# Optimization experiments

Hardware: AMD Instinct MI355X
Metric: run time of the kernel (lower is better)

## Reference

```python
import math
import jax, jax.numpy as jnp
import numpy as np

B, L, C, H = 32, 320, 768, 12
LENS_T = 64
KEEP_RATIO = 0.7
AD_H = 64   # Mixer adapter bottleneck width (assumed bottleneck adapter)
EPS = 1e-5  # torch LayerNorm default


def _ln(x, g, b):
    m = jnp.mean(x, axis=-1, keepdims=True)
    v = jnp.mean((x - m) ** 2, axis=-1, keepdims=True)
    return (x - m) * jax.lax.rsqrt(v + EPS) * g + b


def _attention(x, qkv_w, proj_w, proj_b):
    b, l, c = x.shape
    dh = c // H
    qkv = (x @ qkv_w).reshape(b, l, 3, H, dh)
    q = jnp.transpose(qkv[:, :, 0], (0, 2, 1, 3))  # [B,H,L,Dh]
    k = jnp.transpose(qkv[:, :, 1], (0, 2, 1, 3))
    v = jnp.transpose(qkv[:, :, 2], (0, 2, 1, 3))
    a = jax.nn.softmax(jnp.einsum('bhid,bhjd->bhij', q * (dh ** -0.5), k), axis=-1)
    out = jnp.einsum('bhij,bhjd->bhid', a, v).transpose(0, 2, 1, 3).reshape(b, l, c)
    return out @ proj_w + proj_b, a


def _mixer(x, dw, db, uw, ub):
    return jax.nn.gelu(x @ dw + db, approximate=False) @ uw + ub


def _mlp(x, w1, b1, w2, b2):
    return jax.nn.gelu(x @ w1 + b1, approximate=False) @ w2 + b2


def _ce(attn, tokens, lens_t, lens_keep, gidx):
    # attn: [B,H,Lt+Ls,Lt+Ls]; average template->search block over heads and template rows
    attn_t = jnp.mean(attn[:, :, :lens_t, lens_t:], axis=(1, 2))  # [B, Ls]
    order = jnp.argsort(-attn_t, axis=1)                          # descending sort indices
    topk_idx, rest_idx = order[:, :lens_keep], order[:, lens_keep:]
    keep = jnp.take_along_axis(gidx, topk_idx, axis=1)
    removed = jnp.take_along_axis(gidx, rest_idx, axis=1)
    kept_tok = jnp.take_along_axis(tokens[:, lens_t:], topk_idx[..., None], axis=1)
    return jnp.concatenate([tokens[:, :lens_t], kept_tok], axis=1), keep, removed


def setup_inputs():
    key = jax.random.key(0)
    ks = jax.random.split(key, 12)
    p = lambda k, shape: jax.random.normal(k, shape, jnp.float32) * 0.02
    ls = L - LENS_T
    return {
        'x': jax.random.normal(ks[0], (B, L, C), jnp.float32),
        'xi': jax.random.normal(ks[1], (B, L, C), jnp.float32),
        'gi_t': jnp.arange(B * LENS_T, dtype=jnp.int32).reshape(B, LENS_T),
        'gi_ti': jnp.arange(B * LENS_T, dtype=jnp.int32).reshape(B, LENS_T),
        'gi_s': jnp.arange(B * ls, dtype=jnp.int32).reshape(B, ls),
        'gi_si': jnp.arange(B * ls, dtype=jnp.int32).reshape(B, ls),
        'layer': 0,
        'n1_g': jnp.ones((C,), jnp.float32), 'n1_b': jnp.zeros((C,), jnp.float32),
        'qkv_w': p(ks[2], (C, 3 * C)),
        'proj_w': p(ks[3], (C, C)), 'proj_b': jnp.zeros((C,), jnp.float32),
        'n2_g': jnp.ones((C,), jnp.float32), 'n2_b': jnp.zeros((C,), jnp.float32),
        'fc1_w': p(ks[4], (C, 4 * C)), 'fc1_b': jnp.zeros((4 * C,), jnp.float32),
        'fc2_w': p(ks[5], (4 * C, C)), 'fc2_b': jnp.zeros((C,), jnp.float32),
        'ad1_dw': p(ks[6], (C, AD_H)), 'ad1_db': jnp.zeros((AD_H,), jnp.float32),
        'ad1_uw': p(ks[7], (AD_H, C)), 'ad1_ub': jnp.zeros((C,), jnp.float32),
        'ad2_dw': p(ks[8], (C, AD_H)), 'ad2_db': jnp.zeros((AD_H,), jnp.float32),
        'ad2_uw': p(ks[9], (AD_H, C)), 'ad2_ub': jnp.zeros((C,), jnp.float32),
    }


def reference(x, xi, gi_t, gi_ti, gi_s, gi_si, layer,
              n1_g, n1_b, qkv_w, proj_w, proj_b, n2_g, n2_b,
              fc1_w, fc1_b, fc2_w, fc2_b,
              ad1_dw, ad1_db, ad1_uw, ad1_ub, ad2_dw, ad2_db, ad2_uw, ad2_ub):
    # layer not in {3,6,9}: Mixer-adapter path, then candidate elimination, then MLP
    xori = x
    xa, attn = _attention(_ln(x, n1_g, n1_b), qkv_w, proj_w, proj_b)
    x = x + xa + _mixer(_ln(xi, n1_g, n1_b), ad1_dw, ad1_db, ad1_uw, ad1_ub)
    xia, i_attn = _attention(_ln(xi, n1_g, n1_b), qkv_w, proj_w, proj_b)
    xi = xi + xia + _mixer(_ln(xori, n1_g, n1_b), ad1_dw, ad1_db, ad1_uw, ad1_ub)
    lens_t = gi_t.shape[1]
    lens_s = x.shape[1] - lens_t
    lens_keep = math.ceil(KEEP_RATIO * lens_s)  # 180
    x, gi_s, removed = _ce(attn, x, lens_t, lens_keep, gi_s)
    xi, gi_si, removedi = _ce(i_attn, xi, lens_t, lens_keep, gi_si)
    xori = x
    x = x + _mlp(_ln(x, n2_g, n2_b), fc1_w, fc1_b, fc2_w, fc2_b) \
          + _mixer(_ln(xi, n2_g, n2_b), ad2_dw, ad2_db, ad2_uw, ad2_ub)
    xi = xi + _mlp(_ln(xi, n2_g, n2_b), fc1_w, fc1_b, fc2_w, fc2_b) \
            + _mixer(_ln(xori, n2_g, n2_b), ad2_dw, ad2_db, ad2_uw, ad2_ub)
    return (x, gi_t, gi_s, removed, attn, xi, gi_ti, gi_si, removedi, i_attn)
```

## Files before the change

### kernel.cpp

```cpp
#include <hip/hip_runtime.h>
#include <hip/hip_bf16.h>

#define NB   32
#define LL   320
#define CC   768
#define NH   12
#define DHD  64
#define LT   64
#define LSN  256
#define NKEEP 180
#define NREM  76
#define LP   244
#define ADH  64
#define C4   3072

typedef __attribute__((ext_vector_type(8))) short s16x8;
typedef __attribute__((ext_vector_type(4))) float f32x4;

__device__ __forceinline__ ushort f2b(float f){
  union { __hip_bfloat16 h; ushort u; } cv;
  cv.h = __float2bfloat16(f);
  return cv.u;
}

__device__ __forceinline__ void glds16(const ushort* g, ushort* l){
  __builtin_amdgcn_global_load_lds(
      (const __attribute__((address_space(1))) void*)g,
      (__attribute__((address_space(3))) void*)l, 16, 0, 0);
}

__device__ __forceinline__ float blk_sum(float v, float* sh){
  #pragma unroll
  for (int o = 32; o > 0; o >>= 1) v += __shfl_down(v, o, 64);
  int w = threadIdx.x >> 6;
  if ((threadIdx.x & 63) == 0) sh[w] = v;
  __syncthreads();
  float r = sh[0] + sh[1] + sh[2] + sh[3];
  __syncthreads();
  return r;
}

__global__ __launch_bounds__(256) void ln_k(const float* __restrict__ x,
                                            const float* __restrict__ g,
                                            const float* __restrict__ be,
                                            float* __restrict__ y,
                                            ushort* __restrict__ yb){
  __shared__ float sh[4];
  size_t row = blockIdx.x;
  const float* xr = x + row * CC;
  int t = threadIdx.x;
  float v0 = xr[t], v1 = xr[t + 256], v2 = xr[t + 512];
  float m = blk_sum(v0 + v1 + v2, sh) * (1.0f / 768.0f);
  float d0 = v0 - m, d1 = v1 - m, d2 = v2 - m;
  float var = blk_sum(d0*d0 + d1*d1 + d2*d2, sh) * (1.0f / 768.0f);
  float rs = rsqrtf(var + 1e-5f);
  float o0 = d0 * rs * g[t]       + be[t];
  float o1 = d1 * rs * g[t + 256] + be[t + 256];
  float o2 = d2 * rs * g[t + 512] + be[t + 512];
  float* yr = y + row * CC;
  yr[t] = o0; yr[t + 256] = o1; yr[t + 512] = o2;
  if (yb){
    ushort* yr2 = yb + row * CC;
    yr2[t] = f2b(o0); yr2[t + 256] = f2b(o1); yr2[t + 512] = f2b(o2);
  }
}

__global__ __launch_bounds__(256) void copyt_k(const float* __restrict__ ln1,
                                               float* __restrict__ lnt){
  int row = blockIdx.x;
  int sb = row >> 6, i = row & 63;
  const float* src = ln1 + ((size_t)sb * LL + i) * CC;
  float* dst = lnt + (size_t)row * CC;
  int t = threadIdx.x;
  dst[t] = src[t]; dst[t+256] = src[t+256]; dst[t+512] = src[t+512];
}

__global__ __launch_bounds__(256) void gemm2_k(const float* __restrict__ A,
                                               const float* __restrict__ W,
                                               float* __restrict__ Cm,
                                               ushort* __restrict__ Cb,
                                               int M, int N, int K, int ldw, int ldc){
  __shared__ float As[32][132];
  __shared__ float Bs[32][132];
  const int t = threadIdx.x;
  const int tx = t & 15, ty = t >> 4;
  const int m0 = blockIdx.y * 128, n0 = blockIdx.x * 128;
  float acc[8][8] = {};
  for (int k0 = 0; k0 < K; k0 += 32){
    #pragma unroll
    for (int q = 0; q < 4; q++){
      int idx = t + q*256;
      int m = idx & 127, kq = idx >> 7;
      float4 v = *reinterpret_cast<const float4*>(A + (size_t)(m0+m)*K + k0 + kq*4);
      As[kq*4+0][m] = v.x; As[kq*4+1][m] = v.y;
      As[kq*4+2][m] = v.z; As[kq*4+3][m] = v.w;
    }
    #pragma unroll
    for (int q = 0; q < 4; q++){
      int idx = t + q*256;
      int kr = idx >> 5, nq = idx & 31;
      float4 v = *reinterpret_cast<const float4*>(W + (size_t)(k0+kr)*ldw + n0 + nq*4);
      *reinterpret_cast<float4*>(&Bs[kr][nq*4]) = v;
    }
    __syncthreads();
    #pragma unroll
    for (int kk = 0; kk < 32; kk++){
      float a[8], b[8];
      *reinterpret_cast<float4*>(&a[0]) = *reinterpret_cast<float4*>(&As[kk][ty*4]);
      *reinterpret_cast<float4*>(&a[4]) = *reinterpret_cast<float4*>(&As[kk][64 + ty*4]);
      *reinterpret_cast<float4*>(&b[0]) = *reinterpret_cast<float4*>(&Bs[kk][tx*4]);
      *reinterpret_cast<float4*>(&b[4]) = *reinterpret_cast<float4*>(&Bs[kk][64 + tx*4]);
      #pragma unroll
      for (int i = 0; i < 8; i++)
        #pragma unroll
        for (int j = 0; j < 8; j++)
          acc[i][j] = fmaf(a[i], b[j], acc[i][j]);
    }
    __syncthreads();
  }
  #pragma unroll
  for (int i = 0; i < 8; i++){
    int m = m0 + ty*4 + (i & 3) + (i >> 2) * 64;
    #pragma unroll
    for (int j = 0; j < 8; j++){
      int n = n0 + tx*4 + (j & 3) + (j >> 2) * 64;
      float v = acc[i][j];
      Cm[(size_t)m * ldc + n] = v;
      if (Cb) Cb[(size_t)m * ldc + n] = f2b(v);
    }
  }
}

template<bool GELU, bool ACC, bool OBF>
__global__ __launch_bounds__(256) void mg_k(
    const ushort* __restrict__ A, const ushort* __restrict__ Wt,
    const float* __restrict__ bias, void* __restrict__ Cp,
    int M, int N, int K,
    const float* __restrict__ res0, const float* __restrict__ res1, int Mhalf,
    const ushort* __restrict__ A2_0, const ushort* __restrict__ A2_1,
    const ushort* __restrict__ W2t, int K2, const float* __restrict__ bias2)
{
  __shared__ __align__(16) ushort Asm[128*32];
  __shared__ __align__(16) ushort Bsm[128*32];
  const int t = threadIdx.x;
  const int m0 = blockIdx.y * 128, n0 = blockIdx.x * 128;
  const int wave = t >> 6, lane = t & 63;
  const int wrow = wave >> 1, wcol = wave & 1;
  const int lr = lane & 15, ks = lane >> 4;
  const int srow = lane >> 2, scp = lane & 3;

  f32x4 acc[4][4];
  #pragma unroll
  for (int i = 0; i < 4; i++)
    #pragma unroll
    for (int j = 0; j < 4; j++)
      #pragma unroll
      for (int r = 0; r < 4; r++) acc[i][j][r] = 0.f;

  const int nseg = W2t ? 2 : 1;
  for (int seg = 0; seg < nseg; seg++){
    const ushort* Abase; const ushort* Bbase; int ldA, ldB, Ks;
    if (seg == 0){
      Abase = A + (size_t)m0 * K; ldA = K; Bbase = Wt; ldB = K; Ks = K;
    } else {
      Abase = (res1 && m0 >= Mhalf) ? (A2_1 + (size_t)(m0 - Mhalf) * K2)
                                    : (A2_0 + (size_t)m0 * K2);
      ldA = K2; Bbase = W2t; ldB = K2; Ks = K2;
    }
    for (int k0 = 0; k0 < Ks; k0 += 32){
      #pragma unroll
      for (int q = 0; q < 2; q++){
        int r16 = wave*32 + q*16;
        int row = r16 + srow;
        int sch = scp ^ ((row >> 1) & 3);
        glds16(Abase + (size_t)row * ldA + k0 + sch*8, &Asm[r16*32]);
        int rb = n0 + row; if (rb > N-1) rb = N-1;
        glds16(Bbase + (size_t)rb * ldB + k0 + sch*8, &Bsm[r16*32]);
      }
      __syncthreads();
      s16x8 af[4], bf[4];
      #pragma unroll
      for (int f = 0; f < 4; f++){
        int ra = wrow*64 + f*16 + lr;
        af[f] = *reinterpret_cast<const s16x8*>(&Asm[ra*32 + ((ks ^ ((ra>>1)&3))<<3)]);
        int rb = wcol*64 + f*16 + lr;
        bf[f] = *reinterpret_cast<const s16x8*>(&Bsm[rb*32 + ((ks ^ ((rb>>1)&3))<<3)]);
      }
      #pragma unroll
      for (int i = 0; i < 4; i++)
        #pragma unroll
        for (int j = 0; j < 4; j++)
          acc[i][j] = __builtin_amdgcn_mfma_f32_16x16x32_bf16(af[i], bf[j], acc[i][j], 0, 0, 0);
      __syncthreads();
    }
  }
  #pragma unroll
  for (int i = 0; i < 4; i++){
    int mb = m0 + wrow*64 + i*16 + ks*4;
    #pragma unroll
    for (int j = 0; j < 4; j++){
      int n = n0 + wcol*64 + j*16 + lr;
      if (n >= N) continue;
      float bv = (bias ? bias[n] : 0.0f) + (bias2 ? bias2[n] : 0.0f);
      #pragma unroll
      for (int r = 0; r < 4; r++){
        int mrow = mb + r;
        float v = acc[i][j][r] + bv;
        if (GELU) v = 0.5f * v * (1.0f + erff(v * 0.70710678118654752f));
        if (res0){
          if (res1 && mrow >= Mhalf) v += res1[(size_t)(mrow - Mhalf) * N + n];
          else                       v += res0[(size_t)mrow * N + n];
        }
        size_t idx = (size_t)mrow * N + n;
        if (OBF)      ((ushort*)Cp)[idx] = f2b(v);
        else if (ACC) ((float*)Cp)[idx] += v;
        else          ((float*)Cp)[idx]  = v;
      }
    }
  }
}

__global__ __launch_bounds__(256) void tconv_k(const float* __restrict__ W,
                                               ushort* __restrict__ Wt,
                                               int K, int N, int ldw, int colOff){
  __shared__ float tile[32][33];
  int t = threadIdx.x;
  int tx = t & 31, ty = t >> 5;
  int k0 = blockIdx.y * 32, n0 = blockIdx.x * 32;
  #pragma unroll
  for (int q = 0; q < 4; q++)
    tile[ty + 8*q][tx] = W[(size_t)(k0 + ty + 8*q) * ldw + colOff + n0 + tx];
  __syncthreads();
  #pragma unroll
  for (int q = 0; q < 4; q++)
    Wt[(size_t)(n0 + ty + 8*q) * K + k0 + tx] = f2b(tile[tx][ty + 8*q]);
}

__global__ __launch_bounds__(256) void scorest_k(const float* __restrict__ qt,
                                                 const float* __restrict__ kf,
                                                 float* __restrict__ p0,
                                                 float* __restrict__ p1){
  __shared__ float Qs[16][65];
  __shared__ float Ks[16][65];
  const int t = threadIdx.x, tx = t & 15, ty = t >> 4;
  const int s = blockIdx.y;
  const int bh = blockIdx.z; const int b = bh / NH, h = bh % NH;
  const int j0 = blockIdx.x * 64;
  float* sc = s ? p1 : p0;
  const float* qts = qt + (size_t)s * NB * 64 * CC;
  const float* kfs = kf + (size_t)s * NB * LL * CC;
  const size_t qbase = (size_t)b * 64 * CC + (size_t)h * 64;
  const size_t kbase = (size_t)b * LL * CC + (size_t)h * 64;
  const int lkk = t & 15, lmm = t >> 4;
  float acc[4][4] = {};
  for (int d0 = 0; d0 < DHD; d0 += 16){
    #pragma unroll
    for (int q = 0; q < 4; q++)
      Qs[lkk][lmm + 16*q] = qts[qbase + (size_t)(lmm + 16*q) * CC + d0 + lkk];
    #pragma unroll
    for (int q = 0; q < 4; q++)
      Ks[lkk][lmm + 16*q] = kfs[kbase + (size_t)(j0 + lmm + 16*q) * CC + d0 + lkk];
    __syncthreads();
    #pragma unroll
    for (int kk = 0; kk < 16; kk++){
      float a[4], b2[4];
      #pragma unroll
      for (int i = 0; i < 4; i++) a[i] = Qs[kk][ty*4 + i];
      #pragma unroll
      for (int j = 0; j < 4; j++) b2[j] = Ks[kk][tx*4 + j];
      #pragma unroll
      for (int i = 0; i < 4; i++)
        #pragma unroll
        for (int j = 0; j < 4; j++)
          acc[i][j] = fmaf(a[i], b2[j], acc[i][j]);
    }
    __syncthreads();
  }
  #pragma unroll
  for (int i = 0; i < 4; i++)
    #pragma unroll
    for (int j = 0; j < 4; j++)
      sc[((size_t)bh * LL + ty*4 + i) * LL + j0 + tx*4 + j] = acc[i][j] * 0.125f;
}

__global__ __launch_bounds__(256) void sqs_k(const ushort* __restrict__ qb,
                                             const ushort* __restrict__ kb,
                                             float* __restrict__ p0,
                                             float* __restrict__ p1){
  __shared__ ushort Qs[64][72];
  __shared__ ushort Ks[64][72];
  const int t = threadIdx.x;
  const int it = blockIdx.x, bh = blockIdx.y, s = blockIdx.z;
  const int b = bh / NH, h = bh % NH;
  const int w = t >> 6, lane = t & 63;
  const int lr = lane & 15, ks = lane >> 4;
  float* sc = s ? p1 : p0;
  const ushort* qbs = qb + (size_t)s * NB * LL * CC;
  const ushort* kbs = kb + (size_t)s * NB * LL * CC;
  const int qrow0 = b * LL + 64 + it * 64;

  #pragma unroll
  for (int q = 0; q < 4; q++){
    int idx = t + q*256;
    int row = idx >> 4, dv = idx & 15;
    *reinterpret_cast<ushort4*>(&Qs[row][dv*4]) =
      *reinterpret_cast<const ushort4*>(qbs + (size_t)(qrow0 + row) * CC + h*64 + dv*4);
  }

  f32x4 acc[5][4];
  #pragma unroll
  for (int jt = 0; jt < 5; jt++)
    #pragma unroll
    for (int n = 0; n < 4; n++)
      #pragma unroll
      for (int r = 0; r < 4; r++) acc[jt][n][r] = 0.f;

  for (int jt = 0; jt < 5; jt++){
    __syncthreads();
    #pragma unroll
    for (int q = 0; q < 4; q++){
      int idx = t + q*256;
      int row = idx >> 4, dv = idx & 15;
      *reinterpret_cast<ushort4*>(&Ks[row][dv*4]) =
        *reinterpret_cast<const ushort4*>(kbs + (size_t)(b*LL + jt*64 + row) * CC + h*64 + dv*4);
    }
    __syncthreads();
    #pragma unroll
    for (int n = 0; n < 4; n++)
      #pragma unroll
      for (int kt = 0; kt < 2; kt++){
        s16x8 a  = *reinterpret_cast<const s16x8*>(&Qs[w*16 + lr][kt*32 + ks*8]);
        s16x8 bb = *reinterpret_cast<const s16x8*>(&Ks[n*16 + lr][kt*32 + ks*8]);
        acc[jt][n] = __builtin_amdgcn_mfma_f32_16x16x32_bf16(a, bb, acc[jt][n], 0, 0, 0);
      }
  }
  #pragma unroll
  for (int jt = 0; jt < 5; jt++)
    #pragma unroll
    for (int n = 0; n < 4; n++)
      #pragma unroll
      for (int r = 0; r < 4; r++) acc[jt][n][r] *= 0.125f;
  #pragma unroll
  for (int r = 0; r < 4; r++){
    float mx = -3.4e38f;
    #pragma unroll
    for (int jt = 0; jt < 5; jt++)
      #pragma unroll
      for (int n = 0; n < 4; n++) mx = fmaxf(mx, acc[jt][n][r]);
    #pragma unroll
    for (int o = 1; o < 16; o <<= 1) mx = fmaxf(mx, __shfl_xor(mx, o, 64));
    float sum = 0.f;
    #pragma unroll
    for (int jt = 0; jt < 5; jt++)
      #pragma unroll
      for (int n = 0; n < 4; n++){
        float e = expf(acc[jt][n][r] - mx);
        acc[jt][n][r] = e; sum += e;
      }
    #pragma unroll
    for (int o = 1; o < 16; o <<= 1) sum += __shfl_xor(sum, o, 64);
    float inv = 1.0f / sum;
    size_t rowbase = ((size_t)bh * LL + 64 + it*64 + w*16 + ks*4 + r) * LL;
    #pragma unroll
    for (int jt = 0; jt < 5; jt++)
      #pragma unroll
      for (int n = 0; n < 4; n++)
        sc[rowbase + jt*64 + n*16 + lr] = acc[jt][n][r] * inv;
  }
}

__global__ __launch_bounds__(256) void softmaxt_k(float* __restrict__ p0,
                                                  float* __restrict__ p1){
  const int lane = threadIdx.x & 63;
  const int s = blockIdx.x / (NB*NH*16);
  const int bx = blockIdx.x % (NB*NH*16);
  const int bh = bx >> 4;
  const int i0 = (bx & 15) * 4;
  float* sc = s ? p1 : p0;
  const size_t row = (size_t)bh * LL + i0 + (threadIdx.x >> 6);
  float* sr = sc + row * LL;
  float v[5]; float mx = -3.4e38f;
  #pragma unroll
  for (int i = 0; i < 5; i++){ v[i] = sr[lane + 64*i]; mx = fmaxf(mx, v[i]); }
  #pragma unroll
  for (int o = 32; o > 0; o >>= 1) mx = fmaxf(mx, __shfl_xor(mx, o, 64));
  float s2 = 0.f;
  #pragma unroll
  for (int i = 0; i < 5; i++){ v[i] = expf(v[i] - mx); s2 += v[i]; }
  #pragma unroll
  for (int o = 32; o > 0; o >>= 1) s2 += __shfl_xor(s2, o, 64);
  float inv = 1.0f / s2;
  #pragma unroll
  for (int i = 0; i < 5; i++) sr[lane + 64*i] = v[i] * inv;
}

__global__ __launch_bounds__(256) void attnt1_k(const float* __restrict__ p0,
                                                const float* __restrict__ p1,
                                                double* __restrict__ pp){
  int g = blockIdx.x;
  int s = g / (NB*NH), bh = g % (NB*NH);
  int j = threadIdx.x;
  const float* probs = s ? p1 : p0;
  double sum = 0.0;
  for (int i = 0; i < LT; i++)
    sum += (double)probs[((size_t)bh * LL + i) * LL + 64 + j];
  pp[(size_t)g * LSN + j] = sum;
}
__global__ __launch_bounds__(256) void attnt2_k(const double* __restrict__ pp,
                                                float* __restrict__ at){
  int g = blockIdx.x;
  int j = threadIdx.x;
  double sum = 0.0;
  for (int h = 0; h < NH; h++)
    sum += pp[((size_t)g * NH + h) * LSN + j];
  at[g * LSN + j] = (float)(sum * (1.0 / 768.0));
}

__global__ __launch_bounds__(256) void pvm_k(const float* __restrict__ p0,
                                             const float* __restrict__ p1,
                                             const ushort* __restrict__ vbb,
                                             ushort* __restrict__ pvb){
  __shared__ ushort Pa[64][72];
  __shared__ ushort Vt[64][72];
  const int t = threadIdx.x;
  const int bh = blockIdx.y, s = blockIdx.z;
  const int b = bh / NH, h = bh % NH;
  const int i0 = blockIdx.x * 64;
  const int w = t >> 6, lane = t & 63;
  const int lr = lane & 15, ks = lane >> 4;
  const float* Ap = (s ? p1 : p0) + (size_t)bh * LL * LL;
  const ushort* vbs = vbb + (size_t)s * NB * LL * CC;
  ushort* pvs = pvb + (size_t)s * NB * LL * CC;

  f32x4 acc[4];
  #pragma unroll
  for (int n = 0; n < 4; n++)
    #pragma unroll
    for (int r = 0; r < 4; r++) acc[n][r] = 0.f;

  for (int jt = 0; jt < 5; jt++){
    int j0 = jt * 64;
    #pragma unroll
    for (int q = 0; q < 4; q++){
      int idx = t + q*256;
      int i = idx >> 4, jv = idx & 15;
      float4 v = *reinterpret_cast<const float4*>(Ap + (size_t)(i0 + i) * LL + j0 + jv*4);
      ushort4 u; u.x = f2b(v.x); u.y = f2b(v.y); u.z = f2b(v.z); u.w = f2b(v.w);
      *reinterpret_cast<ushort4*>(&Pa[i][jv*4]) = u;
    }
    #pragma unroll
    for (int q = 0; q < 4; q++){
      int idx = t + q*256;
      int j = idx >> 4, dv = idx & 15;
      ushort4 u = *reinterpret_cast<const ushort4*>(
          vbs + (size_t)(b * LL + j0 + j) * 768 + h*64 + dv*4);
      Vt[dv*4+0][j] = u.x; Vt[dv*4+1][j] = u.y;
      Vt[dv*4+2][j] = u.z; Vt[dv*4+3][j] = u.w;
    }
    __syncthreads();
    #pragma unroll
    for (int n = 0; n < 4; n++)
      #pragma unroll
      for (int kt = 0; kt < 2; kt++){
        s16x8 a = *reinterpret_cast<const s16x8*>(&Pa[w*16 + lr][kt*32 + ks*8]);
        s16x8 bb = *reinterpret_cast<const s16x8*>(&Vt[n*16 + lr][kt*32 + ks*8]);
        acc[n] = __builtin_amdgcn_mfma_f32_16x16x32_bf16(a, bb, acc[n], 0, 0, 0);
      }
    __syncthreads();
  }
  #pragma unroll
  for (int n = 0; n < 4; n++)
    #pragma unroll
    for (int r = 0; r < 4; r++){
      int i = w*16 + ks*4 + r;
      int d = n*16 + lr;
      pvs[(size_t)(b * LL + i0 + i) * 768 + h*64 + d] = f2b(acc[n][r]);
    }
}

__global__ __launch_bounds__(256) void init_ord_k(int* __restrict__ ordbuf, int n){
  int i = blockIdx.x * 256 + threadIdx.x;
  if (i < n) ordbuf[i] = i & 255;
}

__global__ __launch_bounds__(256) void ce_rank_k(const float* __restrict__ at,
                                                 int* __restrict__ ordbuf){
  __shared__ float a[256];
  int b = blockIdx.x, t = threadIdx.x;
  a[t] = at[b * LSN + t];
  __syncthreads();
  float mine = a[t];
  int rank = 0;
  for (int k = 0; k < 256; k++){
    float ak = a[k];
    rank += (ak > mine) || (ak == mine && k < t);
  }
  if (rank >= 0 && rank < 256) ordbuf[b * LSN + rank] = t;
}

__global__ __launch_bounds__(256) void ce_emit_k(const int* __restrict__ ordbuf,
                                                 const int* __restrict__ gidx,
                                                 const int* __restrict__ gt,
                                                 float* __restrict__ out_keep,
                                                 float* __restrict__ out_rem,
                                                 float* __restrict__ out_git){
  int b = blockIdx.x, t = threadIdx.x;
  int o = ordbuf[b * LSN + t];
  o = min(max(o, 0), 255);
  int idx = gidx[b * LSN + o];
  if (t < NKEEP) out_keep[b * NKEEP + t] = (float)idx;
  else           out_rem[b * NREM + (t - NKEEP)] = (float)idx;
  if (t < LT)    out_git[b * LT + t] = (float)gt[b * LT + t];
}

__global__ __launch_bounds__(256) void gather_k(const float* __restrict__ xnew,
                                                const int* __restrict__ ordbuf,
                                                float* __restrict__ x2){
  int g = blockIdx.x;
  int s = g / (NB*LP), r0 = g % (NB*LP);
  int b = r0 / LP, r = r0 % LP;
  int o = (r < LT) ? 0 : ordbuf[(size_t)(s*NB + b) * LSN + (r - LT)];
  o = min(max(o, 0), 255);
  int src = (r < LT) ? r : (LT + o);
  const float* sp = xnew + (size_t)s * NB * LL * CC + ((size_t)b * LL + src) * CC;
  float* d = x2 + (size_t)s * NB * LP * CC + (size_t)r0 * CC;
  for (int i = threadIdx.x; i < CC; i += 256) d[i] = sp[i];
}

__global__ void sentinel_k(float* __restrict__ d, float val, int n){
  int i = blockIdx.x * 256 + threadIdx.x;
  if (i < n) d[i] = val;
}

extern "C" void kernel_launch(void* const* d_in, const int* in_sizes, int n_in,
                              void* d_out, int out_size, void* d_ws, size_t ws_size,
                              hipStream_t stream) {
  float* out = (float*)d_out;
  float* ws  = (float*)d_ws;

  static const int EXP[26] = {
    7864320, 7864320, 2048, 2048, 8192, 8192, 1,
    768, 768, 1769472, 589824, 768, 768, 768,
    2359296, 3072, 2359296, 768,
    49152, 64, 49152, 768, 49152, 64, 49152, 768 };

  const void* P[26];
  bool ok = false;
  if (n_in == 26){
    bool m = true; int bad = -1;
    for (int i = 0; i < 26; i++) if (in_sizes[i] != EXP[i]){ m = false; bad = i; break; }
    if (m){ for (int i = 0; i < 26; i++) P[i] = d_in[i]; ok = true; }
    else { sentinel_k<<<16, 256, 0, stream>>>(out, 20000.0f + 16.0f*bad, 4096); return; }
  } else if (n_in == 25){
    bool m = true; int bad = -1;
    for (int i = 0; i < 25; i++){
      int j = (i < 6) ? i : i + 1;
      if (in_sizes[i] != EXP[j]){ m = false; bad = i; break; }
    }
    if (m){
      for (int j = 0; j < 26; j++) P[j] = (j == 6) ? nullptr : d_in[(j < 6) ? j : j - 1];
      ok = true;
    } else { sentinel_k<<<16, 256, 0, stream>>>(out, 20000.0f + 16.0f*bad, 4096); return; }
  }
  if (!ok){ sentinel_k<<<16, 256, 0, stream>>>(out, 10000.0f + 8.0f*n_in, 4096); return; }
  if (out_size != 90656768){
    sentinel_k<<<16, 256, 0, stream>>>(out, 60000.0f + (float)(out_size / 1000000), 4096); return;
  }

  const float* x      = (const float*)P[0];
  const float* xi     = (const float*)P[1];
  const int*   gi_t   = (const int*)P[2];
  const int*   gi_ti  = (const int*)P[3];
  const int*   gi_s   = (const int*)P[4];
  const int*   gi_si  = (const int*)P[5];
  const float* n1_g   = (const float*)P[7];
  const float* n1_b   = (const float*)P[8];
  const float* qkv_w  = (const float*)P[9];
  const float* proj_w = (const float*)P[10];
  const float* proj_b = (const float*)P[11];
  const float* n2_g   = (const float*)P[12];
  const float* n2_b   = (const float*)P[13];
  const float* fc1_w  = (const float*)P[14];
  const float* fc1_b  = (const float*)P[15];
  const float* fc2_w  = (const float*)P[16];
  const float* fc2_b  = (const float*)P[17];
  const float* ad1_dw = (const float*)P[18];
  const float* ad1_db = (const float*)P[19];
  const float* ad1_uw = (const float*)P[20];
  const float* ad1_ub = (const float*)P[21];
  const float* ad2_dw = (const float*)P[22];
  const float* ad2_db = (const float*)P[23];
  const float* ad2_uw = (const float*)P[24];
  const float* ad2_ub = (const float*)P[25];

  const size_t o_x     = 0;
  const size_t o_git   = 5996544;
  const size_t o_gis   = 5998592;
  const size_t o_rem   = 6004352;
  const size_t o_attn  = 6006784;
  const size_t o_xi    = 45328384;
  const size_t o_giti  = 51324928;
  const size_t o_gisi  = 51326976;
  const size_t o_remi  = 51332736;
  const size_t o_iattn = 51335168;

  const size_t BLC      = (size_t)NB * LL * CC;
  const size_t BPC      = (size_t)NB * LP * CC;
  const size_t off_ln   = 0;
  const size_t off_l1b  = off_ln  + 2*BLC;
  const size_t off_k    = off_l1b + BLC;
  const size_t off_qb   = off_k   + 2*BLC;
  const size_t off_kb   = off_qb  + BLC;
  const size_t off_vb   = off_kb  + BLC;
  const size_t off_lnt  = off_vb  + BLC;
  const size_t off_qt   = off_lnt + 3145728;
  const size_t off_xnew = off_qt  + 3145728;
  const size_t off_l2b  = off_xnew+ 2*BLC;
  const size_t off_mixh = off_l2b + BPC;
  const size_t off_att  = off_mixh+ 655360;
  const size_t off_attp = off_att + 16384;
  const size_t off_ord  = off_attp+ 393216;
  const size_t off_wts  = off_ord + 16384;
  const size_t total_f  = off_wts + 3342336;
  if (ws_size < total_f * sizeof(float)){
    sentinel_k<<<16, 256, 0, stream>>>(out, 40000.0f + (float)(ws_size >> 20), 4096);
    return;
  }

  int* ordbuf = (int*)(ws + off_ord);
  double* attp = (double*)(ws + off_attp);
  ushort* wts = (ushort*)(ws + off_wts);
  ushort* Wt_q    = wts;
  ushort* Wt_v    = wts + 589824;
  ushort* Wt_proj = wts + 1179648;
  ushort* Wt_fc1  = wts + 1769472;
  ushort* Wt_fc2  = wts + 4128768;
  ushort* Wt_a1d  = wts + 6488064;
  ushort* Wt_a1u  = wts + 6537216;
  ushort* Wt_a2d  = wts + 6586368;
  ushort* Wt_a2u  = wts + 6635520;
  ushort* ln1b = (ushort*)(ws + off_l1b);
  ushort* qb   = (ushort*)(ws + off_qb);
  ushort* kb   = (ushort*)(ws + off_kb);
  ushort* vbb  = (ushort*)(ws + off_vb);
  ushort* pvb  = (ushort*)(ws + off_k);
  ushort* ln2b = (ushort*)(ws + off_l2b);
  ushort* mixhb= (ushort*)(ws + off_mixh);

  float* p0 = out + o_attn;
  float* p1 = out + o_iattn;

  tconv_k<<<dim3(24, 24), 256, 0, stream>>>(qkv_w,  Wt_q,    768, 768,  2304, 0);
  tconv_k<<<dim3(24, 24), 256, 0, stream>>>(qkv_w,  Wt_v,    768, 768,  2304, 1536);
  tconv_k<<<dim3(24, 24), 256, 0, stream>>>(proj_w, Wt_proj, 768, 768,  768,  0);
  tconv_k<<<dim3(96, 24), 256, 0, stream>>>(fc1_w,  Wt_fc1,  768, 3072, 3072, 0);
  tconv_k<<<dim3(24, 96), 256, 0, stream>>>(fc2_w,  Wt_fc2,  3072, 768, 768,  0);
  tconv_k<<<dim3(2,  24), 256, 0, stream>>>(ad1_dw, Wt_a1d,  768, 64,   64,   0);
  tconv_k<<<dim3(24, 2 ), 256, 0, stream>>>(ad1_uw, Wt_a1u,  64,  768,  768,  0);
  tconv_k<<<dim3(2,  24), 256, 0, stream>>>(ad2_dw, Wt_a2d,  768, 64,   64,   0);
  tconv_k<<<dim3(24, 2 ), 256, 0, stream>>>(ad2_uw, Wt_a2u,  64,  768,  768,  0);

  ln_k<<<NB*LL, 256, 0, stream>>>(x,  n1_g, n1_b, ws + off_ln,       ln1b);
  ln_k<<<NB*LL, 256, 0, stream>>>(xi, n1_g, n1_b, ws + off_ln + BLC, ln1b + BLC);
  copyt_k<<<2*NB*64, 256, 0, stream>>>(ws + off_ln, ws + off_lnt);
  mg_k<true,false,true><<<dim3(1, 160), 256, 0, stream>>>(
      ln1b, Wt_a1d, ad1_db, mixhb, 2*NB*LL, ADH, CC,
      nullptr, nullptr, 0, nullptr, nullptr, nullptr, 0, nullptr);
  gemm2_k<<<dim3(6, 160), 256, 0, stream>>>(
      ws + off_ln, qkv_w + 768, ws + off_k, kb, 2*NB*LL, CC, CC, 2304, CC);
  gemm2_k<<<dim3(6, 32), 256, 0, stream>>>(
      ws + off_lnt, qkv_w, ws + off_qt, nullptr, 2*NB*64, CC, CC, 2304, CC);
  mg_k<false,false,true><<<dim3(6, 160), 256, 0, stream>>>(
      ln1b, Wt_q, nullptr, qb, 2*NB*LL, CC, CC,
      nullptr, nullptr, 0, nullptr, nullptr, nullptr, 0, nullptr);
  mg_k<false,false,true><<<dim3(6, 160), 256, 0, stream>>>(
      ln1b, Wt_v, nullptr, vbb, 2*NB*LL, CC, CC,
      nullptr, nullptr, 0, nullptr, nullptr, nullptr, 0, nullptr);

  scorest_k<<<dim3(5, 2, NB*NH), 256, 0, stream>>>(ws + off_qt, ws + off_k, p0, p1);
  sqs_k<<<dim3(4, NB*NH, 2), 256, 0, stream>>>(qb, kb, p0, p1);
  softmaxt_k<<<2*NB*NH*16, 256, 0, stream>>>(p0, p1);
  attnt1_k<<<2*NB*NH, 256, 0, stream>>>(p0, p1, attp);
  attnt2_k<<<2*NB, 256, 0, stream>>>(attp, ws + off_att);

  pvm_k<<<dim3(5, NB*NH, 2), 256, 0, stream>>>(p0, p1, vbb, pvb);
  mg_k<false,false,false><<<dim3(6, 160), 256, 0, stream>>>(
      pvb, Wt_proj, proj_b, ws + off_xnew, 2*NB*LL, CC, CC,
      x, xi, NB*LL,
      mixhb + (size_t)NB*LL*ADH, mixhb, Wt_a1u, ADH, ad1_ub);

  init_ord_k<<<(2*NB*LSN + 255)/256, 256, 0, stream>>>(ordbuf, 2*NB*LSN);
  ce_rank_k<<<2*NB, 256, 0, stream>>>(ws + off_att, ordbuf);
  for (int s = 0; s < 2; s++)
    ce_emit_k<<<NB, 256, 0, stream>>>(
        ordbuf + (size_t)s * NB * LSN,
        s ? gi_si : gi_s, s ? gi_ti : gi_t,
        out + (s ? o_gisi : o_gis), out + (s ? o_remi : o_rem),
        out + (s ? o_giti : o_git));
  gather_k<<<2*NB*LP, 256, 0, stream>>>(ws + off_xnew, ordbuf, ws + off_ln);

  float* x2  = ws + off_ln;
  float* ln2 = ws + off_xnew;
  ushort* hidb   = (ushort*)(ws + off_k);
  ushort* mixh2b = mixhb;

  ln_k<<<2*NB*LP, 256, 0, stream>>>(x2, n2_g, n2_b, ln2, ln2b);
  mg_k<true,false,true><<<dim3(1, 122), 256, 0, stream>>>(
      ln2b, Wt_a2d, ad2_db, mixh2b, 2*NB*LP, ADH, CC,
      nullptr, nullptr, 0, nullptr, nullptr, nullptr, 0, nullptr);
  mg_k<true,false,true><<<dim3(24, 122), 256, 0, stream>>>(
      ln2b, Wt_fc1, fc1_b, hidb, 2*NB*LP, C4, CC,
      nullptr, nullptr, 0, nullptr, nullptr, nullptr, 0, nullptr);

  for (int s = 0; s < 2; s++){
    float* xout = out + (s ? o_xi : o_x);
    mg_k<false,false,false><<<dim3(6, 61), 256, 0, stream>>>(
        hidb + (size_t)s * NB * LP * C4, Wt_fc2, fc2_b, xout,
        NB*LP, CC, C4,
        x2 + (size_t)s * BPC, nullptr, 0,
        mixh2b + (size_t)(1 - s) * NB * LP * ADH, nullptr, Wt_a2u, ADH, ad2_ub);
  }
}
```

Measured before the change: 1.456 ms.

## Merge launches: fused Q/V GEMM, combined fp32 GEMMs, LN-template copy, single fc2

```diff
diff --git a/kernel.cpp b/kernel.cpp
--- a/kernel.cpp
+++ b/kernel.cpp
@@ -44,7 +44,8 @@
                                             const float* __restrict__ g,
                                             const float* __restrict__ be,
                                             float* __restrict__ y,
-                                            ushort* __restrict__ yb){
+                                            ushort* __restrict__ yb,
+                                            float* __restrict__ lnt){
   __shared__ float sh[4];
   size_t row = blockIdx.x;
   const float* xr = x + row * CC;
@@ -63,60 +64,71 @@
     ushort* yr2 = yb + row * CC;
     yr2[t] = f2b(o0); yr2[t + 256] = f2b(o1); yr2[t + 512] = f2b(o2);
   }
-}
-
-__global__ __launch_bounds__(256) void copyt_k(const float* __restrict__ ln1,
-                                               float* __restrict__ lnt){
-  int row = blockIdx.x;
-  int sb = row >> 6, i = row & 63;
-  const float* src = ln1 + ((size_t)sb * LL + i) * CC;
-  float* dst = lnt + (size_t)row * CC;
-  int t = threadIdx.x;
-  dst[t] = src[t]; dst[t+256] = src[t+256]; dst[t+512] = src[t+512];
-}
-
-__global__ __launch_bounds__(256) void gemm2_k(const float* __restrict__ A,
-                                               const float* __restrict__ W,
-                                               float* __restrict__ Cm,
-                                               ushort* __restrict__ Cb,
-                                               int M, int N, int K, int ldw, int ldc){
-  __shared__ float As[32][132];
-  __shared__ float Bs[32][132];
+  if (lnt){
+    int i = (int)(row % LL);
+    if (i < 64){
+      float* lr = lnt + ((row / LL) * 64 + i) * CC;
+      lr[t] = o0; lr[t + 256] = o1; lr[t + 512] = o2;
+    }
+  }
+}
+
+__global__ __launch_bounds__(256) void gemm2_k(
+    const float* __restrict__ A1, const float* __restrict__ W1,
+    float* __restrict__ C1, ushort* __restrict__ Cb1,
+    const float* __restrict__ A2, const float* __restrict__ W2,
+    float* __restrict__ C2,
+    int K, int ldw, int ldc, int ysplit)
+{
+  __shared__ float As[32*128];
+  __shared__ float Bs[32*128];
   const int t = threadIdx.x;
   const int tx = t & 15, ty = t >> 4;
-  const int m0 = blockIdx.y * 128, n0 = blockIdx.x * 128;
-  float acc[8][8] = {};
-  for (int k0 = 0; k0 < K; k0 += 32){
+  const int n0 = blockIdx.x * 128;
+  const int yb = blockIdx.y;
+  const float* A; const float* W; float* Cm; ushort* Cb; int m0;
+  if (yb < ysplit){ A = A1; W = W1; Cm = C1; Cb = Cb1; m0 = yb * 128; }
+  else            { A = A2; W = W2; Cm = C2; Cb = nullptr; m0 = (yb - ysplit) * 128; }
+
+  float4 ra[4], rb[4];
+  auto loadT = [&](int k0){
     #pragma unroll
     for (int q = 0; q < 4; q++){
       int idx = t + q*256;
       int m = idx & 127, kq = idx >> 7;
-      float4 v = *reinterpret_cast<const float4*>(A + (size_t)(m0+m)*K + k0 + kq*4);
-      As[kq*4+0][m] = v.x; As[kq*4+1][m] = v.y;
-      As[kq*4+2][m] = v.z; As[kq*4+3][m] = v.w;
-    }
+      ra[q] = *reinterpret_cast<const float4*>(A + (size_t)(m0+m)*K + k0 + kq*4);
+      int kr = idx >> 5, nq = idx & 31;
+      rb[q] = *reinterpret_cast<const float4*>(W + (size_t)(k0+kr)*ldw + n0 + nq*4);
+    }
+  };
+  loadT(0);
+  float acc[8][8] = {};
+  for (int k0 = 0; k0 < K; k0 += 32){
+    __syncthreads();
     #pragma unroll
     for (int q = 0; q < 4; q++){
       int idx = t + q*256;
+      int m = idx & 127, kq = idx >> 7;
+      As[(kq*4+0)*128 + m] = ra[q].x; As[(kq*4+1)*128 + m] = ra[q].y;
+      As[(kq*4+2)*128 + m] = ra[q].z; As[(kq*4+3)*128 + m] = ra[q].w;
       int kr = idx >> 5, nq = idx & 31;
-      float4 v = *reinterpret_cast<const float4*>(W + (size_t)(k0+kr)*ldw + n0 + nq*4);
-      *reinterpret_cast<float4*>(&Bs[kr][nq*4]) = v;
+      *reinterpret_cast<float4*>(&Bs[kr*128 + nq*4]) = rb[q];
     }
     __syncthreads();
+    if (k0 + 32 < K) loadT(k0 + 32);
     #pragma unroll
     for (int kk = 0; kk < 32; kk++){
       float a[8], b[8];
-      *reinterpret_cast<float4*>(&a[0]) = *reinterpret_cast<float4*>(&As[kk][ty*4]);
-      *reinterpret_cast<float4*>(&a[4]) = *reinterpret_cast<float4*>(&As[kk][64 + ty*4]);
-      *reinterpret_cast<float4*>(&b[0]) = *reinterpret_cast<float4*>(&Bs[kk][tx*4]);
-      *reinterpret_cast<float4*>(&b[4]) = *reinterpret_cast<float4*>(&Bs[kk][64 + tx*4]);
+      *reinterpret_cast<float4*>(&a[0]) = *reinterpret_cast<float4*>(&As[kk*128 + ty*4]);
+      *reinterpret_cast<float4*>(&a[4]) = *reinterpret_cast<float4*>(&As[kk*128 + 64 + ty*4]);
+      *reinterpret_cast<float4*>(&b[0]) = *reinterpret_cast<float4*>(&Bs[kk*128 + tx*4]);
+      *reinterpret_cast<float4*>(&b[4]) = *reinterpret_cast<float4*>(&Bs[kk*128 + 64 + tx*4]);
       #pragma unroll
       for (int i = 0; i < 8; i++)
         #pragma unroll
         for (int j = 0; j < 8; j++)
           acc[i][j] = fmaf(a[i], b[j], acc[i][j]);
     }
-    __syncthreads();
   }
   #pragma unroll
   for (int i = 0; i < 8; i++){
@@ -138,7 +150,8 @@
     int M, int N, int K,
     const float* __restrict__ res0, const float* __restrict__ res1, int Mhalf,
     const ushort* __restrict__ A2_0, const ushort* __restrict__ A2_1,
-    const ushort* __restrict__ W2t, int K2, const float* __restrict__ bias2)
+    const ushort* __restrict__ W2t, int K2, const float* __restrict__ bias2,
+    void* __restrict__ Cp1)
 {
   __shared__ __align__(16) ushort Asm[128*32];
   __shared__ __align__(16) ushort Bsm[128*32];
@@ -174,8 +187,8 @@
         int row = r16 + srow;
         int sch = scp ^ ((row >> 1) & 3);
         glds16(Abase + (size_t)row * ldA + k0 + sch*8, &Asm[r16*32]);
-        int rb = n0 + row; if (rb > N-1) rb = N-1;
-        glds16(Bbase + (size_t)rb * ldB + k0 + sch*8, &Bsm[r16*32]);
+        int rbn = n0 + row; if (rbn > N-1) rbn = N-1;
+        glds16(Bbase + (size_t)rbn * ldB + k0 + sch*8, &Bsm[r16*32]);
       }
       __syncthreads();
       s16x8 af[4], bf[4];
@@ -183,8 +196,8 @@
       for (int f = 0; f < 4; f++){
         int ra = wrow*64 + f*16 + lr;
         af[f] = *reinterpret_cast<const s16x8*>(&Asm[ra*32 + ((ks ^ ((ra>>1)&3))<<3)]);
-        int rb = wcol*64 + f*16 + lr;
-        bf[f] = *reinterpret_cast<const s16x8*>(&Bsm[rb*32 + ((ks ^ ((rb>>1)&3))<<3)]);
+        int rbn = wcol*64 + f*16 + lr;
+        bf[f] = *reinterpret_cast<const s16x8*>(&Bsm[rbn*32 + ((ks ^ ((rbn>>1)&3))<<3)]);
       }
       #pragma unroll
       for (int i = 0; i < 4; i++)
@@ -211,10 +224,17 @@
           if (res1 && mrow >= Mhalf) v += res1[(size_t)(mrow - Mhalf) * N + n];
           else                       v += res0[(size_t)mrow * N + n];
         }
-        size_t idx = (size_t)mrow * N + n;
-        if (OBF)      ((ushort*)Cp)[idx] = f2b(v);
-        else if (ACC) ((float*)Cp)[idx] += v;
-        else          ((float*)Cp)[idx]  = v;
+        if (Cp1 && mrow >= Mhalf){
+          size_t idx = (size_t)(mrow - Mhalf) * N + n;
+          if (OBF)      ((ushort*)Cp1)[idx] = f2b(v);
+          else if (ACC) ((float*)Cp1)[idx] += v;
+          else          ((float*)Cp1)[idx]  = v;
+        } else {
+          size_t idx = (size_t)mrow * N + n;
+          if (OBF)      ((ushort*)Cp)[idx] = f2b(v);
+          else if (ACC) ((float*)Cp)[idx] += v;
+          else          ((float*)Cp)[idx]  = v;
+        }
       }
     }
   }
@@ -283,7 +303,7 @@
       sc[((size_t)bh * LL + ty*4 + i) * LL + j0 + tx*4 + j] = acc[i][j] * 0.125f;
 }
 
-__global__ __launch_bounds__(256) void sqs_k(const ushort* __restrict__ qb,
+__global__ __launch_bounds__(256) void sqs_k(const ushort* __restrict__ qv,
                                              const ushort* __restrict__ kb,
                                              float* __restrict__ p0,
                                              float* __restrict__ p1){
@@ -295,16 +315,15 @@
   const int w = t >> 6, lane = t & 63;
   const int lr = lane & 15, ks = lane >> 4;
   float* sc = s ? p1 : p0;
-  const ushort* qbs = qb + (size_t)s * NB * LL * CC;
-  const ushort* kbs = kb + (size_t)s * NB * LL * CC;
-  const int qrow0 = b * LL + 64 + it * 64;
+  const int qrow0 = s * NB * LL + b * LL + 64 + it * 64;
+  const int krow0 = s * NB * LL + b * LL;
 
   #pragma unroll
   for (int q = 0; q < 4; q++){
     int idx = t + q*256;
     int row = idx >> 4, dv = idx & 15;
     *reinterpret_cast<ushort4*>(&Qs[row][dv*4]) =
-      *reinterpret_cast<const ushort4*>(qbs + (size_t)(qrow0 + row) * CC + h*64 + dv*4);
+      *reinterpret_cast<const ushort4*>(qv + (size_t)(qrow0 + row) * 1536 + h*64 + dv*4);
   }
 
   f32x4 acc[5][4];
@@ -322,7 +341,7 @@
       int idx = t + q*256;
       int row = idx >> 4, dv = idx & 15;
       *reinterpret_cast<ushort4*>(&Ks[row][dv*4]) =
-        *reinterpret_cast<const ushort4*>(kbs + (size_t)(b*LL + jt*64 + row) * CC + h*64 + dv*4);
+        *reinterpret_cast<const ushort4*>(kb + (size_t)(krow0 + jt*64 + row) * CC + h*64 + dv*4);
     }
     __syncthreads();
     #pragma unroll
@@ -418,7 +437,7 @@
 
 __global__ __launch_bounds__(256) void pvm_k(const float* __restrict__ p0,
                                              const float* __restrict__ p1,
-                                             const ushort* __restrict__ vbb,
+                                             const ushort* __restrict__ qv,
                                              ushort* __restrict__ pvb){
   __shared__ ushort Pa[64][72];
   __shared__ ushort Vt[64][72];
@@ -429,7 +448,7 @@
   const int w = t >> 6, lane = t & 63;
   const int lr = lane & 15, ks = lane >> 4;
   const float* Ap = (s ? p1 : p0) + (size_t)bh * LL * LL;
-  const ushort* vbs = vbb + (size_t)s * NB * LL * CC;
+  const int vrow0 = s * NB * LL + b * LL;
   ushort* pvs = pvb + (size_t)s * NB * LL * CC;
 
   f32x4 acc[4];
@@ -453,7 +472,7 @@
       int idx = t + q*256;
       int j = idx >> 4, dv = idx & 15;
       ushort4 u = *reinterpret_cast<const ushort4*>(
-          vbs + (size_t)(b * LL + j0 + j) * 768 + h*64 + dv*4);
+          qv + (size_t)(vrow0 + j0 + j) * 1536 + 768 + h*64 + dv*4);
       Vt[dv*4+0][j] = u.x; Vt[dv*4+1][j] = u.y;
       Vt[dv*4+2][j] = u.z; Vt[dv*4+3][j] = u.w;
     }
@@ -498,14 +517,25 @@
   if (rank >= 0 && rank < 256) ordbuf[b * LSN + rank] = t;
 }
 
-__global__ __launch_bounds__(256) void ce_emit_k(const int* __restrict__ ordbuf,
-                                                 const int* __restrict__ gidx,
-                                                 const int* __restrict__ gt,
-                                                 float* __restrict__ out_keep,
-                                                 float* __restrict__ out_rem,
-                                                 float* __restrict__ out_git){
-  int b = blockIdx.x, t = threadIdx.x;
-  int o = ordbuf[b * LSN + t];
+__global__ __launch_bounds__(256) void ce_emit2_k(const int* __restrict__ ordbuf,
+                                                  const int* __restrict__ g0,
+                                                  const int* __restrict__ g1,
+                                                  const int* __restrict__ t0,
+                                                  const int* __restrict__ t1,
+                                                  float* __restrict__ keep0,
+                                                  float* __restrict__ keep1,
+                                                  float* __restrict__ rem0,
+                                                  float* __restrict__ rem1,
+                                                  float* __restrict__ git0,
+                                                  float* __restrict__ git1){
+  int g = blockIdx.x, t = threadIdx.x;
+  int s = g / NB, b = g % NB;
+  const int* gidx = s ? g1 : g0;
+  const int* gt   = s ? t1 : t0;
+  float* out_keep = s ? keep1 : keep0;
+  float* out_rem  = s ? rem1 : rem0;
+  float* out_git  = s ? git1 : git0;
+  int o = ordbuf[(size_t)g * LSN + t];
   o = min(max(o, 0), 255);
   int idx = gidx[b * LSN + o];
   if (t < NKEEP) out_keep[b * NKEEP + t] = (float)idx;
@@ -609,10 +639,9 @@
   const size_t off_ln   = 0;
   const size_t off_l1b  = off_ln  + 2*BLC;
   const size_t off_k    = off_l1b + BLC;
-  const size_t off_qb   = off_k   + 2*BLC;
-  const size_t off_kb   = off_qb  + BLC;
-  const size_t off_vb   = off_kb  + BLC;
-  const size_t off_lnt  = off_vb  + BLC;
+  const size_t off_qv   = off_k   + 2*BLC;
+  const size_t off_kb   = off_qv  + 2*BLC;
+  const size_t off_lnt  = off_kb  + BLC;
   const size_t off_qt   = off_lnt + 3145728;
   const size_t off_xnew = off_qt  + 3145728;
   const size_t off_l2b  = off_xnew+ 2*BLC;
@@ -640,9 +669,8 @@
   ushort* Wt_a2d  = wts + 6586368;
   ushort* Wt_a2u  = wts + 6635520;
   ushort* ln1b = (ushort*)(ws + off_l1b);
-  ushort* qb   = (ushort*)(ws + off_qb);
+  ushort* qvb  = (ushort*)(ws + off_qv);
   ushort* kb   = (ushort*)(ws + off_kb);
-  ushort* vbb  = (ushort*)(ws + off_vb);
   ushort* pvb  = (ushort*)(ws + off_k);
   ushort* ln2b = (ushort*)(ws + off_l2b);
   ushort* mixhb= (ushort*)(ws + off_mixh);
@@ -660,43 +688,39 @@
   tconv_k<<<dim3(2,  24), 256, 0, stream>>>(ad2_dw, Wt_a2d,  768, 64,   64,   0);
   tconv_k<<<dim3(24, 2 ), 256, 0, stream>>>(ad2_uw, Wt_a2u,  64,  768,  768,  0);
 
-  ln_k<<<NB*LL, 256, 0, stream>>>(x,  n1_g, n1_b, ws + off_ln,       ln1b);
-  ln_k<<<NB*LL, 256, 0, stream>>>(xi, n1_g, n1_b, ws + off_ln + BLC, ln1b + BLC);
-  copyt_k<<<2*NB*64, 256, 0, stream>>>(ws + off_ln, ws + off_lnt);
+  ln_k<<<NB*LL, 256, 0, stream>>>(x,  n1_g, n1_b, ws + off_ln, ln1b, ws + off_lnt);
+  ln_k<<<NB*LL, 256, 0, stream>>>(xi, n1_g, n1_b, ws + off_ln + BLC,
+                                  ln1b + (size_t)NB*LL*CC,
+                                  ws + off_lnt + (size_t)NB*64*CC);
   mg_k<true,false,true><<<dim3(1, 160), 256, 0, stream>>>(
       ln1b, Wt_a1d, ad1_db, mixhb, 2*NB*LL, ADH, CC,
-      nullptr, nullptr, 0, nullptr, nullptr, nullptr, 0, nullptr);
-  gemm2_k<<<dim3(6, 160), 256, 0, stream>>>(
-      ws + off_ln, qkv_w + 768, ws + off_k, kb, 2*NB*LL, CC, CC, 2304, CC);
-  gemm2_k<<<dim3(6, 32), 256, 0, stream>>>(
-      ws + off_lnt, qkv_w, ws + off_qt, nullptr, 2*NB*64, CC, CC, 2304, CC);
-  mg_k<false,false,true><<<dim3(6, 160), 256, 0, stream>>>(
-      ln1b, Wt_q, nullptr, qb, 2*NB*LL, CC, CC,
-      nullptr, nullptr, 0, nullptr, nullptr, nullptr, 0, nullptr);
-  mg_k<false,false,true><<<dim3(6, 160), 256, 0, stream>>>(
-      ln1b, Wt_v, nullptr, vbb, 2*NB*LL, CC, CC,
-      nullptr, nullptr, 0, nullptr, nullptr, nullptr, 0, nullptr);
+      nullptr, nullptr, 0, nullptr, nullptr, nullptr, 0, nullptr, nullptr);
+  gemm2_k<<<dim3(6, 192), 256, 0, stream>>>(
+      ws + off_ln, qkv_w + 768, ws + off_k, kb,
+      ws + off_lnt, qkv_w, ws + off_qt,
+      CC, 2304, CC, 160);
+  mg_k<false,false,true><<<dim3(12, 160), 256, 0, stream>>>(
+      ln1b, Wt_q, nullptr, qvb, 2*NB*LL, 1536, CC,
+      nullptr, nullptr, 0, nullptr, nullptr, nullptr, 0, nullptr, nullptr);
 
   scorest_k<<<dim3(5, 2, NB*NH), 256, 0, stream>>>(ws + off_qt, ws + off_k, p0, p1);
-  sqs_k<<<dim3(4, NB*NH, 2), 256, 0, stream>>>(qb, kb, p0, p1);
+  sqs_k<<<dim3(4, NB*NH, 2), 256, 0, stream>>>(qvb, kb, p0, p1);
   softmaxt_k<<<2*NB*NH*16, 256, 0, stream>>>(p0, p1);
   attnt1_k<<<2*NB*NH, 256, 0, stream>>>(p0, p1, attp);
   attnt2_k<<<2*NB, 256, 0, stream>>>(attp, ws + off_att);
 
-  pvm_k<<<dim3(5, NB*NH, 2), 256, 0, stream>>>(p0, p1, vbb, pvb);
+  pvm_k<<<dim3(5, NB*NH, 2), 256, 0, stream>>>(p0, p1, qvb, pvb);
   mg_k<false,false,false><<<dim3(6, 160), 256, 0, stream>>>(
       pvb, Wt_proj, proj_b, ws + off_xnew, 2*NB*LL, CC, CC,
       x, xi, NB*LL,
-      mixhb + (size_t)NB*LL*ADH, mixhb, Wt_a1u, ADH, ad1_ub);
+      mixhb + (size_t)NB*LL*ADH, mixhb, Wt_a1u, ADH, ad1_ub, nullptr);
 
   init_ord_k<<<(2*NB*LSN + 255)/256, 256, 0, stream>>>(ordbuf, 2*NB*LSN);
   ce_rank_k<<<2*NB, 256, 0, stream>>>(ws + off_att, ordbuf);
-  for (int s = 0; s < 2; s++)
-    ce_emit_k<<<NB, 256, 0, stream>>>(
-        ordbuf + (size_t)s * NB * LSN,
-        s ? gi_si : gi_s, s ? gi_ti : gi_t,
-        out + (s ? o_gisi : o_gis), out + (s ? o_remi : o_rem),
-        out + (s ? o_giti : o_git));
+  ce_emit2_k<<<2*NB, 256, 0, stream>>>(
+      ordbuf, gi_s, gi_si, gi_t, gi_ti,
+      out + o_gis, out + o_gisi, out + o_rem, out + o_remi,
+      out + o_git, out + o_giti);
   gather_k<<<2*NB*LP, 256, 0, stream>>>(ws + off_xnew, ordbuf, ws + off_ln);
 
   float* x2  = ws + off_ln;
@@ -704,20 +728,17 @@
   ushort* hidb   = (ushort*)(ws + off_k);
   ushort* mixh2b = mixhb;
 
-  ln_k<<<2*NB*LP, 256, 0, stream>>>(x2, n2_g, n2_b, ln2, ln2b);
+  ln_k<<<2*NB*LP, 256, 0, stream>>>(x2, n2_g, n2_b, ln2, ln2b, nullptr);
   mg_k<true,false,true><<<dim3(1, 122), 256, 0, stream>>>(
       ln2b, Wt_a2d, ad2_db, mixh2b, 2*NB*LP, ADH, CC,
-      nullptr, nullptr, 0, nullptr, nullptr, nullptr, 0, nullptr);
+      nullptr, nullptr, 0, nullptr, nullptr, nullptr, 0, nullptr, nullptr);
   mg_k<true,false,true><<<dim3(24, 122), 256, 0, stream>>>(
       ln2b, Wt_fc1, fc1_b, hidb, 2*NB*LP, C4, CC,
-      nullptr, nullptr, 0, nullptr, nullptr, nullptr, 0, nullptr);
-
-  for (int s = 0; s < 2; s++){
-    float* xout = out + (s ? o_xi : o_x);
-    mg_k<false,false,false><<<dim3(6, 61), 256, 0, stream>>>(
-        hidb + (size_t)s * NB * LP * C4, Wt_fc2, fc2_b, xout,
-        NB*LP, CC, C4,
-        x2 + (size_t)s * BPC, nullptr, 0,
-        mixh2b + (size_t)(1 - s) * NB * LP * ADH, nullptr, Wt_a2u, ADH, ad2_ub);
-  }
-}
+      nullptr, nullptr, 0, nullptr, nullptr, nullptr, 0, nullptr, nullptr);
+
+  mg_k<false,false,false><<<dim3(6, 122), 256, 0, stream>>>(
+      hidb, Wt_fc2, fc2_b, out + o_x, 2*NB*LP, CC, C4,
+      x2, x2 + BPC, NB*LP,
+      mixh2b + (size_t)NB*LP*ADH, mixh2b, Wt_a2u, ADH, ad2_ub,
+      out + o_xi);
+}
```

Result: faster. 1.415 ms (-2.8%).
